# Performance work log

Measured on AMD Instinct MI355X. Metric: run time of the kernel, lower is better.

## Reference

```python
import jax, jax.numpy as jnp
import numpy as np

HEADS = 16
HEAD_DIM = 128
HIDDEN = HEADS * HEAD_DIM  # 2048
B = 4
S = 2048  # max (padded) sequence length


def setup_inputs() -> dict:
    key = jax.random.key(0)
    k1, k2, k3 = jax.random.split(key, 3)
    x = jax.random.normal(k1, (B, S, HIDDEN), dtype=jnp.float32)
    W_qkv = jax.random.normal(k2, (HIDDEN, 3 * HIDDEN), dtype=jnp.float32) * 0.02
    b_qkv = jax.random.normal(k3, (3 * HIDDEN,), dtype=jnp.float32) * 0.02
    # jagged lengths mirroring the source's TOKENS // (i + 1) pattern
    lengths = jnp.array([S // (i + 1) for i in range(B)], dtype=jnp.int64)
    return {"x": x, "W_qkv": W_qkv, "b_qkv": b_qkv, "lengths": lengths}


def reference(x, W_qkv, b_qkv, lengths):
    # x: [B, S, HIDDEN] padded jagged batch; lengths: [B] valid token counts
    qkv = x @ W_qkv + b_qkv                       # [B, S, 3*HIDDEN]
    q, k, v = jnp.split(qkv, 3, axis=-1)          # each [B, S, HIDDEN]

    def to_heads(t):  # [B, S, HIDDEN] -> [B, H, S, D]
        return t.reshape(B, S, HEADS, HEAD_DIM).transpose(0, 2, 1, 3)

    q, k, v = to_heads(q), to_heads(k), to_heads(v)

    scale = 1.0 / jnp.sqrt(jnp.asarray(HEAD_DIM, dtype=q.dtype))
    scores = jnp.einsum('bhqd,bhkd->bhqk', q, k) * scale  # [B, H, S, S]

    valid = jnp.arange(S)[None, :] < lengths[:, None]     # [B, S]
    neg = jnp.asarray(-1e30, dtype=scores.dtype)
    scores = jnp.where(valid[:, None, None, :], scores, neg)

    attn = jax.nn.softmax(scores, axis=-1)                # [B, H, S, S]
    out = jnp.einsum('bhqk,bhkd->bhqd', attn, v)          # [B, H, S, D]
    # zero out padded query rows (they don't exist in the nested tensor)
    out = out * valid[:, None, :, None].astype(out.dtype)
    return out
```

## Files before the change

kernel.cpp:

```cpp
#include <hip/hip_runtime.h>
#include <stdint.h>

#define BATCH 4
#define SEQ   2048
#define NH    16
#define HD    128
#define HID   2048
#define N3    6144

typedef _Float16 f16;
typedef _Float16 f16x8 __attribute__((ext_vector_type(8)));
typedef _Float16 f16x4 __attribute__((ext_vector_type(4)));
typedef float    f32x4 __attribute__((ext_vector_type(4)));

#define QSCALE 0.1275313895f

__device__ __forceinline__ int get_len(const int* L, int b) {
  return (L[1] == 0) ? L[2 * b] : L[b];
}

__device__ __forceinline__ void async_copy16(void* lds_uniform, const void* gptr) {
  __builtin_amdgcn_global_load_lds(
      (const __attribute__((address_space(1))) void*)(uintptr_t)gptr,
      (__attribute__((address_space(3))) void*)(uint32_t)(uintptr_t)lds_uniform,
      16, 0, 0);
}

__global__ __launch_bounds__(256) void cvt_fused(const float* __restrict__ x,
                                                 f16* __restrict__ xh,
                                                 const float* __restrict__ W,
                                                 f16* __restrict__ Wt) {
  __shared__ float tile[64][65];
  if (blockIdx.x < 8192) {
    int idx = blockIdx.x * 256 + threadIdx.x;
    int m = idx >> 8;
    int g = idx & 255;
    int p = (g & ~3) | ((g ^ ((m >> 1) & 3)) & 3);
    const float* src = x + (size_t)m * HID + g * 8;
    f16x8 o;
#pragma unroll
    for (int j = 0; j < 8; ++j) o[j] = (f16)src[j];
    *(f16x8*)&xh[(size_t)m * HID + p * 8] = o;
  } else {
    int bid = blockIdx.x - 8192;
    const int n0 = (bid % 96) * 64;
    const int k0 = (bid / 96) * 64;
    const int tid = threadIdx.x;
#pragma unroll
    for (int i = 0; i < 4; ++i) {
      int id = tid + i * 256;
      int kr = id >> 4, nc = id & 15;
      f32x4 v = *(const f32x4*)&W[(size_t)(k0 + kr) * N3 + n0 + nc * 4];
#pragma unroll
      for (int j = 0; j < 4; ++j) tile[kr][nc * 4 + j] = v[j];
    }
    __syncthreads();
#pragma unroll
    for (int i = 0; i < 2; ++i) {
      int id = tid + i * 256;
      int nl = id >> 3;
      int kc = id & 7;
      f16x8 o;
#pragma unroll
      for (int j = 0; j < 8; ++j) o[j] = (f16)tile[kc * 8 + j][nl];
      int n = n0 + nl;
      int gk = (k0 >> 3) + kc;
      int p = (gk & ~3) | ((gk ^ ((n >> 1) & 3)) & 3);
      *(f16x8*)&Wt[(size_t)n * HID + p * 8] = o;
    }
  }
}

__global__ __launch_bounds__(256, 3)
void qkv_gemm(const f16* __restrict__ xh, const f16* __restrict__ Wt,
              const float* __restrict__ bias, const int* __restrict__ lens,
              f16* __restrict__ Qh, f16* __restrict__ Kh, f16* __restrict__ Vt) {
  __shared__ f16 As[2 * 128 * 32];
  __shared__ f16 Bs[2 * 128 * 32];

  const int tid = threadIdx.x;
  const int wave = tid >> 6, lane = tid & 63;
  const int lr = lane & 15, quad = lane >> 4;
  const int nblk = blockIdx.x;
  const int mblk = blockIdx.y;
  const int m0 = mblk * 128;
  const int b = m0 >> 11;
  const int s0 = m0 & (SEQ - 1);
  const int len = get_len(lens, b);
  if (s0 >= len) return;
  const int n0 = nblk * 128;
  const int wr = (wave >> 1) * 64;
  const int wc = (wave & 1) * 64;

  f32x4 acc[4][4] = {};
  const char* xbase = (const char*)xh + (size_t)m0 * (HID * 2);
  const char* wbase = (const char*)Wt + (size_t)n0 * (HID * 2);

  for (int k0 = 0; k0 < HID; k0 += 64) {
    __syncthreads();
#pragma unroll
    for (int i = 0; i < 4; ++i) {
      int slot = wave * 4 + i;
      int hh = slot >> 3;
      int sub = slot & 7;
      int row = sub * 16 + (lane >> 2);
      size_t gcol = (size_t)k0 * 2 + hh * 64 + (lane & 3) * 16;
      async_copy16(&As[slot * 512], xbase + (size_t)row * (HID * 2) + gcol);
      async_copy16(&Bs[slot * 512], wbase + (size_t)row * (HID * 2) + gcol);
    }
    __syncthreads();

#pragma unroll
    for (int hh = 0; hh < 2; ++hh) {
      f16x8 a[4], bf[4];
#pragma unroll
      for (int mt = 0; mt < 4; ++mt) {
        int row = wr + mt * 16 + lr;
        int c = quad ^ ((row >> 1) & 3);
        a[mt] = *(const f16x8*)&As[hh * 4096 + row * 32 + c * 8];
      }
#pragma unroll
      for (int nt = 0; nt < 4; ++nt) {
        int row = wc + nt * 16 + lr;
        int c = quad ^ ((row >> 1) & 3);
        bf[nt] = *(const f16x8*)&Bs[hh * 4096 + row * 32 + c * 8];
      }
#pragma unroll
      for (int mt = 0; mt < 4; ++mt)
#pragma unroll
        for (int nt = 0; nt < 4; ++nt)
          acc[mt][nt] = __builtin_amdgcn_mfma_f32_16x16x32_f16(a[mt], bf[nt],
                                                               acc[mt][nt], 0, 0, 0);
    }
  }

  const int t = nblk >> 4;
  const int h = nblk & 15;
  const size_t bhoff = (size_t)(b * NH + h);

  if (t == 0) {
    f16* qp = Qh + bhoff * (SEQ * HD);
#pragma unroll
    for (int nt = 0; nt < 4; ++nt) {
      int d = wc + nt * 16 + lr;
      float bv = bias[n0 + d];
#pragma unroll
      for (int mt = 0; mt < 4; ++mt) {
        int sb = s0 + wr + mt * 16 + quad * 4;
#pragma unroll
        for (int r = 0; r < 4; ++r)
          qp[(size_t)(sb + r) * HD + d] = (f16)((acc[mt][nt][r] + bv) * QSCALE);
      }
    }
  } else if (t == 1) {
    f16* kp = Kh + bhoff * (SEQ * HD);
#pragma unroll
    for (int nt = 0; nt < 4; ++nt) {
      int d = wc + nt * 16 + lr;
      float bv = bias[n0 + d];
#pragma unroll
      for (int mt = 0; mt < 4; ++mt) {
        int sb = s0 + wr + mt * 16 + quad * 4;
#pragma unroll
        for (int r = 0; r < 4; ++r) {
          int s = sb + r;
          int c = (d >> 3) ^ (s & 15);
          kp[(size_t)s * HD + c * 8 + (d & 7)] = (f16)(acc[mt][nt][r] + bv);
        }
      }
    }
  } else {
    f16* vp = Vt + bhoff * (HD * SEQ);
#pragma unroll
    for (int nt = 0; nt < 4; ++nt) {
      int d = wc + nt * 16 + lr;
      float bv = bias[n0 + d];
#pragma unroll
      for (int mt = 0; mt < 4; ++mt) {
        int sb = s0 + wr + mt * 16 + quad * 4;
        f16x4 pk;
#pragma unroll
        for (int r = 0; r < 4; ++r) pk[r] = (f16)(acc[mt][nt][r] + bv);
        int p = (sb >> 3) ^ (d & 7);
        *(f16x4*)&vp[(size_t)d * SEQ + p * 8 + (sb & 7)] = pk;
      }
    }
  }
}

__global__ __launch_bounds__(512, 4)
void attn(const f16* __restrict__ Qh, const f16* __restrict__ Kh,
          const f16* __restrict__ Vt, const int* __restrict__ lens,
          float* __restrict__ out) {
  __shared__ f16 Ks[64 * 128];
  __shared__ f16 Vs[128 * 64];
  __shared__ f16 Ps[128 * 72];

  const int tid = threadIdx.x, wave = tid >> 6, lane = tid & 63;
  const int lr = lane & 15, quad = lane >> 4;
  const int id = blockIdx.x;
  const int bhlo = id & 7;
  const int r3 = id >> 3;
  const int qt = r3 & 15;
  const int bh = ((r3 >> 4) << 3) | bhlo;
  const int b = bh >> 4, h = bh & 15;
  const int len = get_len(lens, b);
  const int q0 = qt * 128;
  const size_t bho = (size_t)(b * NH + h);
  float* obase = out + bho * (size_t)(SEQ * HD);

  if (q0 >= len) {
    f32x4 z = {0.f, 0.f, 0.f, 0.f};
#pragma unroll
    for (int i = 0; i < 8; ++i) {
      int idx = tid + i * 512;
      *(f32x4*)&obase[(size_t)q0 * HD + (size_t)idx * 4] = z;
    }
    return;
  }

  f16x8 qa[4];
  {
    const f16* qp = Qh + bho * (size_t)(SEQ * HD);
    int row = q0 + wave * 16 + lr;
#pragma unroll
    for (int ks = 0; ks < 4; ++ks)
      qa[ks] = *(const f16x8*)&qp[(size_t)row * HD + ks * 32 + quad * 8];
  }

  float lrow[4] = {0.f, 0.f, 0.f, 0.f};
  f32x4 oacc[8] = {};

  const char* kpl = (const char*)(Kh + bho * (size_t)(SEQ * HD));
  const char* vpl = (const char*)(Vt + bho * (size_t)(HD * SEQ));

  const int nkt = (len + 63) >> 6;

  f16x8 kpre[2], vpre[2];
  const int kslot0 = wave * 2;
  const int kkey = (lane >> 4);
  const int kcol = (lane & 15);
  const int vdr = (lane >> 3);
  const int vcol = (lane & 7);

#pragma unroll
  for (int i = 0; i < 2; ++i) {
    int slot = kslot0 + i;
    kpre[i] = *(const f16x8*)(kpl + ((size_t)(slot * 4 + kkey) * HD + kcol * 8) * 2);
    vpre[i] = *(const f16x8*)(vpl + ((size_t)(slot * 8 + vdr) * SEQ + vcol * 8) * 2);
  }

  for (int kt = 0; kt < nkt; ++kt) {
    __syncthreads();
#pragma unroll
    for (int i = 0; i < 2; ++i) {
      int slot = kslot0 + i;
      *(f16x8*)&Ks[slot * 512 + lane * 8] = kpre[i];
      *(f16x8*)&Vs[slot * 512 + lane * 8] = vpre[i];
    }
    __syncthreads();
    if (kt + 1 < nkt) {
      size_t koff = (size_t)(kt + 1) * 64;
#pragma unroll
      for (int i = 0; i < 2; ++i) {
        int slot = kslot0 + i;
        kpre[i] = *(const f16x8*)(kpl + ((koff + slot * 4 + kkey) * HD + kcol * 8) * 2);
        vpre[i] = *(const f16x8*)(vpl + ((size_t)(slot * 8 + vdr) * SEQ + koff + vcol * 8) * 2);
      }
    }

    f32x4 sacc[4] = {};
#pragma unroll
    for (int ks = 0; ks < 4; ++ks) {
      f16x8 kb[4];
#pragma unroll
      for (int nt = 0; nt < 4; ++nt) {
        int key = nt * 16 + lr;
        int c = (ks * 4 + quad) ^ (key & 15);
        kb[nt] = *(const f16x8*)&Ks[key * 128 + c * 8];
      }
#pragma unroll
      for (int nt = 0; nt < 4; ++nt)
        sacc[nt] = __builtin_amdgcn_mfma_f32_16x16x32_f16(qa[ks], kb[nt],
                                                          sacc[nt], 0, 0, 0);
    }

    const int kbase = kt * 64;
    if (kbase + 64 > len) {
#pragma unroll
      for (int nt = 0; nt < 4; ++nt)
        if (kbase + nt * 16 + lr >= len)
#pragma unroll
          for (int r = 0; r < 4; ++r) sacc[nt][r] = -3.0e38f;
    }

#pragma unroll
    for (int nt = 0; nt < 4; ++nt)
#pragma unroll
      for (int r = 0; r < 4; ++r)
        sacc[nt][r] = __builtin_amdgcn_exp2f(sacc[nt][r]);
#pragma unroll
    for (int r = 0; r < 4; ++r)
      lrow[r] += (sacc[0][r] + sacc[1][r]) + (sacc[2][r] + sacc[3][r]);

#pragma unroll
    for (int nt = 0; nt < 4; ++nt)
#pragma unroll
      for (int r = 0; r < 4; ++r)
        Ps[(wave * 16 + quad * 4 + r) * 72 + nt * 16 + lr] = (f16)sacc[nt][r];

#pragma unroll
    for (int ks = 0; ks < 2; ++ks) {
      f16x8 pa = *(const f16x8*)&Ps[(wave * 16 + lr) * 72 + ks * 32 + quad * 8];
#pragma unroll
      for (int nt = 0; nt < 8; ++nt) {
        int d = nt * 16 + lr;
        int c = (ks * 4 + quad) ^ (d & 7);
        f16x8 vb = *(const f16x8*)&Vs[d * 64 + c * 8];
        oacc[nt] = __builtin_amdgcn_mfma_f32_16x16x32_f16(pa, vb, oacc[nt],
                                                          0, 0, 0);
      }
    }
  }

#pragma unroll
  for (int r = 0; r < 4; ++r) {
    float l = lrow[r];
    l += __shfl_xor(l, 1);
    l += __shfl_xor(l, 2);
    l += __shfl_xor(l, 4);
    l += __shfl_xor(l, 8);
    lrow[r] = 1.0f / l;
  }
  {
    int sb = q0 + wave * 16 + quad * 4;
#pragma unroll
    for (int nt = 0; nt < 8; ++nt) {
      int d = nt * 16 + lr;
#pragma unroll
      for (int r = 0; r < 4; ++r) {
        int s = sb + r;
        obase[(size_t)s * HD + d] =
            (s < len) ? oacc[nt][r] * lrow[r] : 0.0f;
      }
    }
  }
}

extern "C" void kernel_launch(void* const* d_in, const int* in_sizes, int n_in,
                              void* d_out, int out_size, void* d_ws, size_t ws_size,
                              hipStream_t stream) {
  const float* x = (const float*)d_in[0];
  const float* W = (const float*)d_in[1];
  const float* bias = (const float*)d_in[2];
  const int* lens = (const int*)d_in[3];
  float* out = (float*)d_out;

  char* ws = (char*)d_ws;
  size_t off = 0;
  f16* xh = (f16*)(ws + off); off += (size_t)BATCH * SEQ * HID * 2;
  f16* Wt = (f16*)(ws + off); off += (size_t)N3 * HID * 2;
  f16* Qh = (f16*)(ws + off); off += (size_t)BATCH * NH * SEQ * HD * 2;
  f16* Kh = (f16*)(ws + off); off += (size_t)BATCH * NH * SEQ * HD * 2;
  f16* Vt = (f16*)(ws + off); off += (size_t)BATCH * NH * SEQ * HD * 2;

  cvt_fused<<<8192 + 3072, 256, 0, stream>>>(x, xh, W, Wt);
  qkv_gemm<<<dim3(48, 64), 256, 0, stream>>>(xh, Wt, bias, lens, Qh, Kh, Vt);
  attn<<<1024, 512, 0, stream>>>(Qh, Kh, Vt, lens, out);
}
```

Measured before the change: 348.9 us.

## Stream GEMM B operand from registers and double attention rows per wave

The QKV GEMM no longer stages W in shared memory. Each wave loads its B fragments straight from global memory into registers, with a one-step register prefetch, so the W swizzle is removed. The grid order is swapped so M blocks vary fastest. The attention kernel drops to 256 threads, with each wave handling 32 query rows (two M tiles) so every K/V tile in LDS is reused twice, and the K/V prefetch is moved after the softmax. This cuts LDS traffic and barrier count but raises register pressure and makes uncoalesced global loads for W.

Measured after the change: 823.4 us. 2.36x slower.

```diff
diff --git a/kernel.cpp b/kernel.cpp
--- a/kernel.cpp
+++ b/kernel.cpp
@@ -63,10 +63,7 @@
       f16x8 o;
 #pragma unroll
       for (int j = 0; j < 8; ++j) o[j] = (f16)tile[kc * 8 + j][nl];
-      int n = n0 + nl;
-      int gk = (k0 >> 3) + kc;
-      int p = (gk & ~3) | ((gk ^ ((n >> 1) & 3)) & 3);
-      *(f16x8*)&Wt[(size_t)n * HID + p * 8] = o;
+      *(f16x8*)&Wt[(size_t)(n0 + nl) * HID + (size_t)k0 + kc * 8] = o;
     }
   }
 }
@@ -76,13 +73,12 @@
               const float* __restrict__ bias, const int* __restrict__ lens,
               f16* __restrict__ Qh, f16* __restrict__ Kh, f16* __restrict__ Vt) {
   __shared__ f16 As[2 * 128 * 32];
-  __shared__ f16 Bs[2 * 128 * 32];
 
   const int tid = threadIdx.x;
   const int wave = tid >> 6, lane = tid & 63;
   const int lr = lane & 15, quad = lane >> 4;
-  const int nblk = blockIdx.x;
-  const int mblk = blockIdx.y;
+  const int mblk = blockIdx.x;
+  const int nblk = blockIdx.y;
   const int m0 = mblk * 128;
   const int b = m0 >> 11;
   const int s0 = m0 & (SEQ - 1);
@@ -94,7 +90,12 @@
 
   f32x4 acc[4][4] = {};
   const char* xbase = (const char*)xh + (size_t)m0 * (HID * 2);
-  const char* wbase = (const char*)Wt + (size_t)n0 * (HID * 2);
+  const f16* wb = Wt + (size_t)n0 * HID;
+
+  f16x8 bn[4];
+#pragma unroll
+  for (int nt = 0; nt < 4; ++nt)
+    bn[nt] = *(const f16x8*)&wb[(size_t)(wc + nt * 16 + lr) * HID + quad * 8];
 
   for (int k0 = 0; k0 < HID; k0 += 64) {
     __syncthreads();
@@ -104,15 +105,23 @@
       int hh = slot >> 3;
       int sub = slot & 7;
       int row = sub * 16 + (lane >> 2);
-      size_t gcol = (size_t)k0 * 2 + hh * 64 + (lane & 3) * 16;
-      async_copy16(&As[slot * 512], xbase + (size_t)row * (HID * 2) + gcol);
-      async_copy16(&Bs[slot * 512], wbase + (size_t)row * (HID * 2) + gcol);
+      async_copy16(&As[slot * 512],
+                   xbase + (size_t)row * (HID * 2) + k0 * 2 + hh * 64 + (lane & 3) * 16);
     }
     __syncthreads();
 
 #pragma unroll
     for (int hh = 0; hh < 2; ++hh) {
-      f16x8 a[4], bf[4];
+      f16x8 bc[4];
+#pragma unroll
+      for (int nt = 0; nt < 4; ++nt) bc[nt] = bn[nt];
+      int kn = k0 + hh * 32 + 32;
+      if (kn < HID) {
+#pragma unroll
+        for (int nt = 0; nt < 4; ++nt)
+          bn[nt] = *(const f16x8*)&wb[(size_t)(wc + nt * 16 + lr) * HID + kn + quad * 8];
+      }
+      f16x8 a[4];
 #pragma unroll
       for (int mt = 0; mt < 4; ++mt) {
         int row = wr + mt * 16 + lr;
@@ -120,16 +129,10 @@
         a[mt] = *(const f16x8*)&As[hh * 4096 + row * 32 + c * 8];
       }
 #pragma unroll
-      for (int nt = 0; nt < 4; ++nt) {
-        int row = wc + nt * 16 + lr;
-        int c = quad ^ ((row >> 1) & 3);
-        bf[nt] = *(const f16x8*)&Bs[hh * 4096 + row * 32 + c * 8];
-      }
-#pragma unroll
       for (int mt = 0; mt < 4; ++mt)
 #pragma unroll
         for (int nt = 0; nt < 4; ++nt)
-          acc[mt][nt] = __builtin_amdgcn_mfma_f32_16x16x32_f16(a[mt], bf[nt],
+          acc[mt][nt] = __builtin_amdgcn_mfma_f32_16x16x32_f16(a[mt], bc[nt],
                                                                acc[mt][nt], 0, 0, 0);
     }
   }
@@ -188,7 +191,7 @@
   }
 }
 
-__global__ __launch_bounds__(512, 4)
+__global__ __launch_bounds__(256, 3)
 void attn(const f16* __restrict__ Qh, const f16* __restrict__ Kh,
           const f16* __restrict__ Vt, const int* __restrict__ lens,
           float* __restrict__ out) {
@@ -212,39 +215,42 @@
   if (q0 >= len) {
     f32x4 z = {0.f, 0.f, 0.f, 0.f};
 #pragma unroll
-    for (int i = 0; i < 8; ++i) {
-      int idx = tid + i * 512;
+    for (int i = 0; i < 16; ++i) {
+      int idx = tid + i * 256;
       *(f32x4*)&obase[(size_t)q0 * HD + (size_t)idx * 4] = z;
     }
     return;
   }
 
-  f16x8 qa[4];
+  f16x8 qa[2][4];
   {
     const f16* qp = Qh + bho * (size_t)(SEQ * HD);
-    int row = q0 + wave * 16 + lr;
-#pragma unroll
-    for (int ks = 0; ks < 4; ++ks)
-      qa[ks] = *(const f16x8*)&qp[(size_t)row * HD + ks * 32 + quad * 8];
-  }
-
-  float lrow[4] = {0.f, 0.f, 0.f, 0.f};
-  f32x4 oacc[8] = {};
+#pragma unroll
+    for (int mt = 0; mt < 2; ++mt) {
+      int row = q0 + wave * 32 + mt * 16 + lr;
+#pragma unroll
+      for (int ks = 0; ks < 4; ++ks)
+        qa[mt][ks] = *(const f16x8*)&qp[(size_t)row * HD + ks * 32 + quad * 8];
+    }
+  }
+
+  float lrow[2][4] = {};
+  f32x4 oacc[2][8] = {};
 
   const char* kpl = (const char*)(Kh + bho * (size_t)(SEQ * HD));
   const char* vpl = (const char*)(Vt + bho * (size_t)(HD * SEQ));
 
   const int nkt = (len + 63) >> 6;
 
-  f16x8 kpre[2], vpre[2];
-  const int kslot0 = wave * 2;
+  f16x8 kpre[4], vpre[4];
+  const int kslot0 = wave * 4;
   const int kkey = (lane >> 4);
   const int kcol = (lane & 15);
   const int vdr = (lane >> 3);
   const int vcol = (lane & 7);
 
 #pragma unroll
-  for (int i = 0; i < 2; ++i) {
+  for (int i = 0; i < 4; ++i) {
     int slot = kslot0 + i;
     kpre[i] = *(const f16x8*)(kpl + ((size_t)(slot * 4 + kkey) * HD + kcol * 8) * 2);
     vpre[i] = *(const f16x8*)(vpl + ((size_t)(slot * 8 + vdr) * SEQ + vcol * 8) * 2);
@@ -253,23 +259,14 @@
   for (int kt = 0; kt < nkt; ++kt) {
     __syncthreads();
 #pragma unroll
-    for (int i = 0; i < 2; ++i) {
+    for (int i = 0; i < 4; ++i) {
       int slot = kslot0 + i;
       *(f16x8*)&Ks[slot * 512 + lane * 8] = kpre[i];
       *(f16x8*)&Vs[slot * 512 + lane * 8] = vpre[i];
     }
     __syncthreads();
-    if (kt + 1 < nkt) {
-      size_t koff = (size_t)(kt + 1) * 64;
-#pragma unroll
-      for (int i = 0; i < 2; ++i) {
-        int slot = kslot0 + i;
-        kpre[i] = *(const f16x8*)(kpl + ((koff + slot * 4 + kkey) * HD + kcol * 8) * 2);
-        vpre[i] = *(const f16x8*)(vpl + ((size_t)(slot * 8 + vdr) * SEQ + koff + vcol * 8) * 2);
-      }
-    }
-
-    f32x4 sacc[4] = {};
+
+    f32x4 sacc[2][4] = {};
 #pragma unroll
     for (int ks = 0; ks < 4; ++ks) {
       f16x8 kb[4];
@@ -280,9 +277,11 @@
         kb[nt] = *(const f16x8*)&Ks[key * 128 + c * 8];
       }
 #pragma unroll
-      for (int nt = 0; nt < 4; ++nt)
-        sacc[nt] = __builtin_amdgcn_mfma_f32_16x16x32_f16(qa[ks], kb[nt],
-                                                          sacc[nt], 0, 0, 0);
+      for (int mt = 0; mt < 2; ++mt)
+#pragma unroll
+        for (int nt = 0; nt < 4; ++nt)
+          sacc[mt][nt] = __builtin_amdgcn_mfma_f32_16x16x32_f16(
+              qa[mt][ks], kb[nt], sacc[mt][nt], 0, 0, 0);
     }
 
     const int kbase = kt * 64;
@@ -291,49 +290,77 @@
       for (int nt = 0; nt < 4; ++nt)
         if (kbase + nt * 16 + lr >= len)
 #pragma unroll
-          for (int r = 0; r < 4; ++r) sacc[nt][r] = -3.0e38f;
-    }
-
-#pragma unroll
-    for (int nt = 0; nt < 4; ++nt)
+          for (int mt = 0; mt < 2; ++mt)
+#pragma unroll
+            for (int r = 0; r < 4; ++r) sacc[mt][nt][r] = -3.0e38f;
+    }
+
+#pragma unroll
+    for (int mt = 0; mt < 2; ++mt) {
+#pragma unroll
+      for (int nt = 0; nt < 4; ++nt)
+#pragma unroll
+        for (int r = 0; r < 4; ++r)
+          sacc[mt][nt][r] = __builtin_amdgcn_exp2f(sacc[mt][nt][r]);
 #pragma unroll
       for (int r = 0; r < 4; ++r)
-        sacc[nt][r] = __builtin_amdgcn_exp2f(sacc[nt][r]);
-#pragma unroll
-    for (int r = 0; r < 4; ++r)
-      lrow[r] += (sacc[0][r] + sacc[1][r]) + (sacc[2][r] + sacc[3][r]);
-
-#pragma unroll
-    for (int nt = 0; nt < 4; ++nt)
-#pragma unroll
-      for (int r = 0; r < 4; ++r)
-        Ps[(wave * 16 + quad * 4 + r) * 72 + nt * 16 + lr] = (f16)sacc[nt][r];
+        lrow[mt][r] += (sacc[mt][0][r] + sacc[mt][1][r]) +
+                       (sacc[mt][2][r] + sacc[mt][3][r]);
+    }
+
+#pragma unroll
+    for (int mt = 0; mt < 2; ++mt)
+#pragma unroll
+      for (int nt = 0; nt < 4; ++nt)
+#pragma unroll
+        for (int r = 0; r < 4; ++r)
+          Ps[(wave * 32 + mt * 16 + quad * 4 + r) * 72 + nt * 16 + lr] =
+              (f16)sacc[mt][nt][r];
+
+    if (kt + 1 < nkt) {
+      size_t koff = (size_t)(kt + 1) * 64;
+#pragma unroll
+      for (int i = 0; i < 4; ++i) {
+        int slot = kslot0 + i;
+        kpre[i] = *(const f16x8*)(kpl + ((koff + slot * 4 + kkey) * HD + kcol * 8) * 2);
+        vpre[i] = *(const f16x8*)(vpl + ((size_t)(slot * 8 + vdr) * SEQ + koff + vcol * 8) * 2);
+      }
+    }
 
 #pragma unroll
     for (int ks = 0; ks < 2; ++ks) {
-      f16x8 pa = *(const f16x8*)&Ps[(wave * 16 + lr) * 72 + ks * 32 + quad * 8];
+      f16x8 pa[2];
+#pragma unroll
+      for (int mt = 0; mt < 2; ++mt)
+        pa[mt] = *(const f16x8*)&Ps[(wave * 32 + mt * 16 + lr) * 72 +
+                                    ks * 32 + quad * 8];
 #pragma unroll
       for (int nt = 0; nt < 8; ++nt) {
         int d = nt * 16 + lr;
         int c = (ks * 4 + quad) ^ (d & 7);
         f16x8 vb = *(const f16x8*)&Vs[d * 64 + c * 8];
-        oacc[nt] = __builtin_amdgcn_mfma_f32_16x16x32_f16(pa, vb, oacc[nt],
-                                                          0, 0, 0);
-      }
-    }
-  }
-
-#pragma unroll
-  for (int r = 0; r < 4; ++r) {
-    float l = lrow[r];
-    l += __shfl_xor(l, 1);
-    l += __shfl_xor(l, 2);
-    l += __shfl_xor(l, 4);
-    l += __shfl_xor(l, 8);
-    lrow[r] = 1.0f / l;
-  }
-  {
-    int sb = q0 + wave * 16 + quad * 4;
+#pragma unroll
+        for (int mt = 0; mt < 2; ++mt)
+          oacc[mt][nt] = __builtin_amdgcn_mfma_f32_16x16x32_f16(
+              pa[mt], vb, oacc[mt][nt], 0, 0, 0);
+      }
+    }
+  }
+
+#pragma unroll
+  for (int mt = 0; mt < 2; ++mt)
+#pragma unroll
+    for (int r = 0; r < 4; ++r) {
+      float l = lrow[mt][r];
+      l += __shfl_xor(l, 1);
+      l += __shfl_xor(l, 2);
+      l += __shfl_xor(l, 4);
+      l += __shfl_xor(l, 8);
+      lrow[mt][r] = 1.0f / l;
+    }
+#pragma unroll
+  for (int mt = 0; mt < 2; ++mt) {
+    int sb = q0 + wave * 32 + mt * 16 + quad * 4;
 #pragma unroll
     for (int nt = 0; nt < 8; ++nt) {
       int d = nt * 16 + lr;
@@ -341,7 +368,7 @@
       for (int r = 0; r < 4; ++r) {
         int s = sb + r;
         obase[(size_t)s * HD + d] =
-            (s < len) ? oacc[nt][r] * lrow[r] : 0.0f;
+            (s < len) ? oacc[mt][nt][r] * lrow[mt][r] : 0.0f;
       }
     }
   }
@@ -365,6 +392,6 @@
   f16* Vt = (f16*)(ws + off); off += (size_t)BATCH * NH * SEQ * HD * 2;
 
   cvt_fused<<<8192 + 3072, 256, 0, stream>>>(x, xh, W, Wt);
-  qkv_gemm<<<dim3(48, 64), 256, 0, stream>>>(xh, Wt, bias, lens, Qh, Kh, Vt);
-  attn<<<1024, 512, 0, stream>>>(Qh, Kh, Vt, lens, out);
-}
+  qkv_gemm<<<dim3(64, 48), 256, 0, stream>>>(xh, Wt, bias, lens, Qh, Kh, Vt);
+  attn<<<1024, 256, 0, stream>>>(Qh, Kh, Vt, lens, out);
+}
```
